# Kernel optimization log

Measured on AMD Instinct MI355X. Metric: run time of the kernel, lower is better.

The kernel has to match this reference:

```python
import jax, jax.numpy as jnp
import numpy as np

B_COEF = 0.1          # position-offset scale 'b'
STRIDE = (1, 1)
PADDING = (1, 1)


def setup_inputs() -> dict:
    key = jax.random.key(0)
    k1, k2, k3 = jax.random.split(key, 3)
    x = jax.random.normal(k1, (16, 64, 128, 128), dtype=jnp.float32)
    kernel = jax.random.normal(k2, (128, 64, 3, 3), dtype=jnp.float32)
    bias = jax.random.normal(k3, (128,), dtype=jnp.float32)
    return {"x": x, "kernel": kernel, "bias": bias}


def _conv(inp, w):
    pads = [(PADDING[0], PADDING[0]), (PADDING[1], PADDING[1])]
    return jax.lax.conv_general_dilated(
        inp, w, window_strides=STRIDE, padding=pads,
        dimension_numbers=("NCHW", "OIHW", "NCHW"))


def reference(x, kernel, bias):
    # out[b,o,p] = sum_i x_unf[b,i,p] * (kernel_flat[o,i] + b*grid[p]) + bias[o]
    # = conv(x, kernel) + b*grid[p] * sum_i x_unf[b,i,p] + bias  (rank-1 separable)
    kh, kw = kernel.shape[2], kernel.shape[3]
    main = _conv(x, kernel)                                  # (B, O, Ho, Wo)
    H_out, W_out = main.shape[2], main.shape[3]

    # sum over in_channels and kernel window = ones-conv of channel-summed input
    ones_k = jnp.ones((1, 1, kh, kw), dtype=x.dtype)
    patch_sum = _conv(x.sum(axis=1, keepdims=True), ones_k)  # (B, 1, Ho, Wo)

    # Replicate torch meshgrid(arange(W_out), arange(H_out), indexing='ij')
    # -> flatten (W,H) row-major -> consumed as (H,W) row-major by the view.
    gx = jnp.arange(W_out)[:, None] + jnp.arange(H_out)[None, :]  # (Wo, Ho)
    grid2d = gx.reshape(-1).reshape(H_out, W_out).astype(x.dtype)  # (Ho, Wo)

    return main + B_COEF * grid2d * patch_sum + bias[None, :, None, None]
```

## Files before the change

### kernel.cpp

```cpp
#include <hip/hip_runtime.h>
#include <hip/hip_bf16.h>


typedef __attribute__((ext_vector_type(8))) short short8;
typedef __attribute__((ext_vector_type(4))) float f32x4;

#define B_COEF 0.1f
constexpr int CI = 64, CO = 128, H = 128, W = 128;
constexpr int SH = 4;
constexpr int XPAD = 72;

static __device__ inline short bf16s(float v) {
    __hip_bfloat16 b = __float2bfloat16(v);
    return *reinterpret_cast<short*>(&b);
}

static __device__ inline void bar_lgkm() {
    asm volatile("s_waitcnt lgkmcnt(0)" ::: "memory");
    __builtin_amdgcn_s_barrier();
    asm volatile("" ::: "memory");
}
static __device__ inline void bar_plain() {
    asm volatile("" ::: "memory");
    __builtin_amdgcn_s_barrier();
    asm volatile("" ::: "memory");
}


__global__ void prep_wq(const float* __restrict__ wgt, __hip_bfloat16* __restrict__ wq) {
    int idx = blockIdx.x * 256 + threadIdx.x;
    if (idx < 9 * CO * CI) {
        int tap = idx >> 13;
        int rem = idx & 8191;
        int oc = rem >> 6, ci = rem & 63;
        int kc = ci >> 5, j = ci & 31;
        wq[(((tap * 2 + kc) * CO + oc) << 5) + j] =
            __float2bfloat16(wgt[(oc * CI + ci) * 9 + tap]);
    }
}

static __device__ __forceinline__ void loadrow(const float* __restrict__ xb, int r,
                                               int wl, int cg0, float* pf) {
    if ((unsigned)r < (unsigned)H) {
        const float* px = xb + (size_t)r * W + wl;
#pragma unroll
        for (int p = 0; p < 4; ++p) {
            const int cg = cg0 + 2 * p;
#pragma unroll
            for (int j = 0; j < 8; ++j)
                pf[p * 8 + j] = px[(size_t)(cg * 8 + j) * (H * W)];
        }
    } else {
#pragma unroll
        for (int i = 0; i < 32; ++i) pf[i] = 0.0f;
    }
}

static __device__ __forceinline__ void writerow(__hip_bfloat16* __restrict__ xs,
                                                float* __restrict__ psb, int tid,
                                                int wslot, int cg0, const float* pf) {
    const int wsw = wslot & 7;
    float part = 0.0f;
#pragma unroll
    for (int p = 0; p < 4; ++p) {
        const int cg = cg0 + 2 * p;
        short8 pk;
#pragma unroll
        for (int j = 0; j < 8; ++j) {
            pk[j] = bf16s(pf[p * 8 + j]);
            part += pf[p * 8 + j];
        }
        *(short8*)&xs[wslot * 64 + ((cg ^ wsw) * 8)] = pk;
    }
    psb[tid] = part;
}

__global__ __launch_bounds__(256, 2)
void conv_fused(const float* __restrict__ x,
                const __hip_bfloat16* __restrict__ wq,
                const float* __restrict__ bias,
                float* __restrict__ out) {
    __shared__ __hip_bfloat16 xrow[3][130 * 64];
    __shared__ float Srow[3][132];
    __shared__ float ps3[132];
    __shared__ float psb[256];

    const int tid = threadIdx.x, bx = blockIdx.x, b = blockIdx.y;
    const int u = ((bx & 7) << 2) | (bx >> 3);
    const int h0 = u * SH;
    const int lane = tid & 63, waveid = tid >> 6;
    const int lo16 = lane & 15, quad = lane >> 4;
    const int m0 = (waveid & 1) * 64, n0 = (waveid >> 1) * 64;
    const int wl = tid & 127, cg0 = tid >> 7, wslot = wl + 1;

    const float* xb = x + (size_t)b * CI * H * W;

    if (tid < 48) {
        const int sl = tid >> 4, col = (tid & 8) ? 129 : 0, uu = tid & 7;
        short8 z = {0, 0, 0, 0, 0, 0, 0, 0};
        *(short8*)&xrow[sl][col * 64 + ((uu ^ (col & 7)) * 8)] = z;
    }
    if (tid == 48) ps3[0] = 0.0f;
    if (tid == 49) ps3[129] = 0.0f;

#pragma unroll
    for (int k = 0; k < 2; ++k) {
        const int r = h0 - 1 + k;
        float pf[32];
        loadrow(xb, r, wl, cg0, pf);
        writerow(&xrow[(r + 1) % 3][0], psb, tid, wslot, cg0, pf);
        bar_lgkm();
        if (tid < 128) Srow[(r + 1) % 3][tid + 1] = psb[tid] + psb[tid + 128];
        bar_lgkm();
    }
    {
        float pf[32];
        loadrow(xb, h0 + 1, wl, cg0, pf);
        writerow(&xrow[(h0 + 2) % 3][0], psb, tid, wslot, cg0, pf);
        bar_lgkm();
    }

    for (int t = 0; t < SH; ++t) {
        const int h = h0 + t;

        float pf[32];
        if (t < SH - 1) loadrow(xb, h + 2, wl, cg0, pf);

        if (tid < 128) {
            const float v = psb[tid] + psb[tid + 128];
            Srow[(h + 2) % 3][tid + 1] = v;
            ps3[tid + 1] = Srow[h % 3][tid + 1] + Srow[(h + 1) % 3][tid + 1] + v;
        }
        bar_lgkm();

        f32x4 acc[4][4] = {};
        __builtin_amdgcn_s_setprio(1);
#pragma unroll
        for (int kh = 0; kh < 3; ++kh) {
            const __hip_bfloat16* xs = &xrow[(h + kh) % 3][0];
#pragma unroll
            for (int kw = 0; kw < 3; ++kw) {
                const int tap = kh * 3 + kw;
                short8 bq[2][4];
#pragma unroll
                for (int kc = 0; kc < 2; ++kc)
#pragma unroll
                    for (int ni = 0; ni < 4; ++ni)
                        bq[kc][ni] = *(const short8*)(
                            wq + (((tap * 2 + kc) * CO + n0 + ni * 16 + lo16) << 5) + quad * 8);
#pragma unroll
                for (int kc = 0; kc < 2; ++kc) {
                    short8 af[4];
#pragma unroll
                    for (int mi = 0; mi < 4; ++mi) {
                        const int row = m0 + mi * 16 + lo16 + kw;
                        af[mi] = *(const short8*)
                            &xs[row * 64 + (((kc * 4 + quad) ^ (row & 7)) * 8)];
                    }
#pragma unroll
                    for (int mi = 0; mi < 4; ++mi)
#pragma unroll
                        for (int ni = 0; ni < 4; ++ni)
                            acc[mi][ni] = __builtin_amdgcn_mfma_f32_16x16x32_bf16(
                                af[mi], bq[kc][ni], acc[mi][ni], 0, 0, 0);
                }
            }
        }
        __builtin_amdgcn_s_setprio(0);

#pragma unroll
        for (int mi = 0; mi < 4; ++mi) {
            const int wbase = m0 + mi * 16 + quad * 4;
            float cs[6];
#pragma unroll
            for (int q2 = 0; q2 < 6; ++q2) cs[q2] = ps3[wbase + q2];
            float ps[4], cf[4];
#pragma unroll
            for (int q2 = 0; q2 < 4; ++q2) {
                ps[q2] = cs[q2] + cs[q2 + 1] + cs[q2 + 2];
                cf[q2] = B_COEF * (float)(h + wbase + q2);
            }
#pragma unroll
            for (int ni = 0; ni < 4; ++ni) {
                const int oc = n0 + ni * 16 + lo16;
                const float bv = bias[oc];
                f32x4 v = acc[mi][ni];
#pragma unroll
                for (int q2 = 0; q2 < 4; ++q2) v[q2] = v[q2] + cf[q2] * ps[q2] + bv;
                *(f32x4*)(out + (((size_t)b * CO + oc) * H + h) * W + wbase) = v;
            }
        }
        bar_plain();

        if (t < SH - 1) {
            writerow(&xrow[h % 3][0], psb, tid, wslot, cg0, pf);
            bar_lgkm();
        }
    }
}


constexpr int WPAD = 72;

__global__ void prep_w_fb(const float* __restrict__ wgt, __hip_bfloat16* __restrict__ wt) {
    int idx = blockIdx.x * 256 + threadIdx.x;
    if (idx < 9 * CO * CI) {
        int tap = idx / (CO * CI);
        int rem = idx - tap * (CO * CI);
        int oc = rem >> 6, ci = rem & 63;
        wt[idx] = __float2bfloat16(wgt[(oc * CI + ci) * 9 + tap]);
    }
}

__global__ __launch_bounds__(256, 2)
void conv_fb(const float* __restrict__ x, const __hip_bfloat16* __restrict__ wt,
             const float* __restrict__ bias, float* __restrict__ out) {
    __shared__ __hip_bfloat16 xrow[130 * XPAD];
    __shared__ __hip_bfloat16 wlds[CO * WPAD];
    __shared__ float colsum[132];

    const int tid = threadIdx.x;
    const int h = blockIdx.x, b = blockIdx.y;
    const int lane = tid & 63, waveid = tid >> 6;
    const int lo16 = lane & 15, quad = lane >> 4;
    const int m0 = (waveid & 1) * 64, n0 = (waveid >> 1) * 64;

    f32x4 acc[4][4] = {};
    if (tid < 132) colsum[tid] = 0.0f;
    const float* xb = x + (size_t)b * CI * H * W;

    const int w16 = tid & 15, cipl = (tid >> 4) & 3, rest0 = tid >> 6;

    for (int kh = 0; kh < 3; ++kh) {
        const int gh = h - 1 + kh;
        __syncthreads();
        for (int it = 0; it < 18; ++it) {
            int rest = rest0 + it * 4;
            int whi = rest % 9, ciph = rest / 9;
            int w = whi * 16 + w16;
            int ci0 = (ciph * 4 + cipl) * 2;
            int gw = w - 1;
            float x0 = 0.0f, x1 = 0.0f;
            if (w < 130 && gw >= 0 && gw < W && gh >= 0 && gh < H) {
                const float* p = xb + (size_t)ci0 * (H * W) + gh * W + gw;
                x0 = p[0];
                x1 = p[H * W];
            }
            if (w < 130) {
                __hip_bfloat162 pk;
                pk.x = __float2bfloat16(x0);
                pk.y = __float2bfloat16(x1);
                *(__hip_bfloat162*)&xrow[w * XPAD + ci0] = pk;
            }
            float cs = x0 + x1;
            cs += __shfl_xor(cs, 16);
            cs += __shfl_xor(cs, 32);
            if (quad == 0 && w < 130) atomicAdd(&colsum[w], cs);
        }
        for (int kw = 0; kw < 3; ++kw) {
            __syncthreads();
            {
                const __hip_bfloat16* wtap = wt + (kh * 3 + kw) * (CO * CI);
#pragma unroll
                for (int it = 0; it < 4; ++it) {
                    int j = tid + it * 256;
                    int oc = j >> 3, ch = (j & 7) * 8;
                    short8 v = *(const short8*)(wtap + oc * CI + ch);
                    *(short8*)&wlds[oc * WPAD + ch] = v;
                }
            }
            __syncthreads();
#pragma unroll
            for (int kc = 0; kc < 2; ++kc) {
                const int krow = kc * 32 + quad * 8;
                short8 af[4], bf[4];
#pragma unroll
                for (int mi = 0; mi < 4; ++mi)
                    af[mi] = *(const short8*)&xrow[(m0 + mi * 16 + lo16 + kw) * XPAD + krow];
#pragma unroll
                for (int ni = 0; ni < 4; ++ni)
                    bf[ni] = *(const short8*)&wlds[(n0 + ni * 16 + lo16) * WPAD + krow];
#pragma unroll
                for (int mi = 0; mi < 4; ++mi)
#pragma unroll
                    for (int ni = 0; ni < 4; ++ni)
                        acc[mi][ni] = __builtin_amdgcn_mfma_f32_16x16x32_bf16(
                            af[mi], bf[ni], acc[mi][ni], 0, 0, 0);
            }
        }
    }
    __syncthreads();
#pragma unroll
    for (int mi = 0; mi < 4; ++mi) {
        const int wbase = m0 + mi * 16 + quad * 4;
        float cs[6];
#pragma unroll
        for (int r = 0; r < 6; ++r) cs[r] = colsum[wbase + r];
        float ps[4], cf[4];
#pragma unroll
        for (int r = 0; r < 4; ++r) {
            ps[r] = cs[r] + cs[r + 1] + cs[r + 2];
            cf[r] = B_COEF * (float)(h + wbase + r);
        }
#pragma unroll
        for (int ni = 0; ni < 4; ++ni) {
            const int oc = n0 + ni * 16 + lo16;
            const float bv = bias[oc];
            f32x4 v = acc[mi][ni];
#pragma unroll
            for (int r = 0; r < 4; ++r) v[r] = v[r] + cf[r] * ps[r] + bv;
            *(f32x4*)(out + (((size_t)b * CO + oc) * H + h) * W + wbase) = v;
        }
    }
}


extern "C" void kernel_launch(void* const* d_in, const int* in_sizes, int n_in,
                              void* d_out, int out_size, void* d_ws, size_t ws_size,
                              hipStream_t stream) {
    const float* x    = (const float*)d_in[0];
    const float* wgt  = (const float*)d_in[1];
    const float* bias = (const float*)d_in[2];
    float* out = (float*)d_out;

    const size_t WQ_BYTES = (size_t)9 * 2 * CO * 32 * 2;

    if (ws_size >= WQ_BYTES) {
        __hip_bfloat16* wq = (__hip_bfloat16*)d_ws;
        prep_wq<<<dim3(288), dim3(256), 0, stream>>>(wgt, wq);
        conv_fused<<<dim3(H / SH, 16), dim3(256), 0, stream>>>(x, wq, bias, out);
    } else {
        __hip_bfloat16* wt = (__hip_bfloat16*)d_ws;
        prep_w_fb<<<dim3(288), dim3(256), 0, stream>>>(wgt, wt);
        conv_fb<<<dim3(H, 16), dim3(256), 0, stream>>>(x, wt, bias, out);
    }
}
```

Baseline: 258.2 us.

## Double workgroup width, split output channels per wave, and deepen row-buffer pipeline

```diff
diff --git a/kernel.cpp b/kernel.cpp
--- a/kernel.cpp
+++ b/kernel.cpp
@@ -17,11 +17,6 @@
 
 static __device__ inline void bar_lgkm() {
     asm volatile("s_waitcnt lgkmcnt(0)" ::: "memory");
-    __builtin_amdgcn_s_barrier();
-    asm volatile("" ::: "memory");
-}
-static __device__ inline void bar_plain() {
-    asm volatile("" ::: "memory");
     __builtin_amdgcn_s_barrier();
     asm volatile("" ::: "memory");
 }
@@ -40,112 +35,115 @@
 }
 
 static __device__ __forceinline__ void loadrow(const float* __restrict__ xb, int r,
-                                               int wl, int cg0, float* pf) {
+                                               int wl, int u0, float* pf) {
     if ((unsigned)r < (unsigned)H) {
         const float* px = xb + (size_t)r * W + wl;
 #pragma unroll
-        for (int p = 0; p < 4; ++p) {
-            const int cg = cg0 + 2 * p;
+        for (int uu = 0; uu < 2; ++uu)
 #pragma unroll
             for (int j = 0; j < 8; ++j)
-                pf[p * 8 + j] = px[(size_t)(cg * 8 + j) * (H * W)];
-        }
+                pf[uu * 8 + j] = px[(size_t)((u0 + uu) * 8 + j) * (H * W)];
     } else {
 #pragma unroll
-        for (int i = 0; i < 32; ++i) pf[i] = 0.0f;
+        for (int i = 0; i < 16; ++i) pf[i] = 0.0f;
     }
 }
 
 static __device__ __forceinline__ void writerow(__hip_bfloat16* __restrict__ xs,
                                                 float* __restrict__ psb, int tid,
-                                                int wslot, int cg0, const float* pf) {
+                                                int wslot, int u0, const float* pf) {
     const int wsw = wslot & 7;
     float part = 0.0f;
 #pragma unroll
-    for (int p = 0; p < 4; ++p) {
-        const int cg = cg0 + 2 * p;
+    for (int uu = 0; uu < 2; ++uu) {
         short8 pk;
 #pragma unroll
         for (int j = 0; j < 8; ++j) {
-            pk[j] = bf16s(pf[p * 8 + j]);
-            part += pf[p * 8 + j];
-        }
-        *(short8*)&xs[wslot * 64 + ((cg ^ wsw) * 8)] = pk;
+            pk[j] = bf16s(pf[uu * 8 + j]);
+            part += pf[uu * 8 + j];
+        }
+        *(short8*)&xs[wslot * 64 + (((u0 + uu) ^ wsw) * 8)] = pk;
     }
     psb[tid] = part;
 }
 
-__global__ __launch_bounds__(256, 2)
+__global__ __launch_bounds__(512, 2)
 void conv_fused(const float* __restrict__ x,
                 const __hip_bfloat16* __restrict__ wq,
                 const float* __restrict__ bias,
                 float* __restrict__ out) {
-    __shared__ __hip_bfloat16 xrow[3][130 * 64];
-    __shared__ float Srow[3][132];
+    __shared__ __hip_bfloat16 xrow[4][130 * 64];
+    __shared__ float Srow[4][132];
     __shared__ float ps3[132];
-    __shared__ float psb[256];
+    __shared__ float psb[512];
 
     const int tid = threadIdx.x, bx = blockIdx.x, b = blockIdx.y;
     const int u = ((bx & 7) << 2) | (bx >> 3);
     const int h0 = u * SH;
     const int lane = tid & 63, waveid = tid >> 6;
     const int lo16 = lane & 15, quad = lane >> 4;
-    const int m0 = (waveid & 1) * 64, n0 = (waveid >> 1) * 64;
-    const int wl = tid & 127, cg0 = tid >> 7, wslot = wl + 1;
+    const int m0 = (waveid & 1) * 64, n0 = (waveid >> 1) * 32;
+    const int wl = tid & 127, u0 = (tid >> 7) * 2, wslot = wl + 1;
 
     const float* xb = x + (size_t)b * CI * H * W;
 
-    if (tid < 48) {
+    if (tid < 64) {
         const int sl = tid >> 4, col = (tid & 8) ? 129 : 0, uu = tid & 7;
         short8 z = {0, 0, 0, 0, 0, 0, 0, 0};
         *(short8*)&xrow[sl][col * 64 + ((uu ^ (col & 7)) * 8)] = z;
     }
-    if (tid == 48) ps3[0] = 0.0f;
-    if (tid == 49) ps3[129] = 0.0f;
-
-#pragma unroll
-    for (int k = 0; k < 2; ++k) {
+    if (tid == 64) ps3[0] = 0.0f;
+    if (tid == 65) ps3[129] = 0.0f;
+
+    float pr0[16], pr1[16], pr2[16], pfA[16], pfB[16];
+    loadrow(xb, h0 - 1, wl, u0, pr0);
+    loadrow(xb, h0,     wl, u0, pr1);
+    loadrow(xb, h0 + 1, wl, u0, pr2);
+    loadrow(xb, h0 + 2, wl, u0, pfA);
+#pragma unroll
+    for (int k = 0; k < 3; ++k) {
         const int r = h0 - 1 + k;
-        float pf[32];
-        loadrow(xb, r, wl, cg0, pf);
-        writerow(&xrow[(r + 1) % 3][0], psb, tid, wslot, cg0, pf);
+        const float* pk = (k == 0) ? pr0 : (k == 1) ? pr1 : pr2;
+        writerow(&xrow[(r + 1) & 3][0], psb, tid, wslot, u0, pk);
         bar_lgkm();
-        if (tid < 128) Srow[(r + 1) % 3][tid + 1] = psb[tid] + psb[tid + 128];
+        if (tid < 128)
+            Srow[(r + 1) & 3][tid + 1] =
+                psb[tid] + psb[tid + 128] + psb[tid + 256] + psb[tid + 384];
         bar_lgkm();
     }
-    {
-        float pf[32];
-        loadrow(xb, h0 + 1, wl, cg0, pf);
-        writerow(&xrow[(h0 + 2) % 3][0], psb, tid, wslot, cg0, pf);
-        bar_lgkm();
-    }
-
+
+#pragma unroll
     for (int t = 0; t < SH; ++t) {
         const int h = h0 + t;
 
-        float pf[32];
-        if (t < SH - 1) loadrow(xb, h + 2, wl, cg0, pf);
-
-        if (tid < 128) {
-            const float v = psb[tid] + psb[tid + 128];
-            Srow[(h + 2) % 3][tid + 1] = v;
-            ps3[tid + 1] = Srow[h % 3][tid + 1] + Srow[(h + 1) % 3][tid + 1] + v;
-        }
+        if (t == 0) loadrow(xb, h0 + 3, wl, u0, pfB);
+        if (t == 1) loadrow(xb, h0 + 4, wl, u0, pfA);
+
+        if (tid < 128)
+            ps3[tid + 1] = Srow[h & 3][tid + 1] + Srow[(h + 1) & 3][tid + 1] +
+                           Srow[(h + 2) & 3][tid + 1];
+
+        if (t < 3)
+            writerow(&xrow[(h + 3) & 3][0], psb, tid, wslot, u0,
+                     (t & 1) ? pfB : pfA);
         bar_lgkm();
-
-        f32x4 acc[4][4] = {};
+        if (t < 3 && tid < 128)
+            Srow[(h + 3) & 3][tid + 1] =
+                psb[tid] + psb[tid + 128] + psb[tid + 256] + psb[tid + 384];
+
+        f32x4 acc[4][2] = {};
         __builtin_amdgcn_s_setprio(1);
 #pragma unroll
         for (int kh = 0; kh < 3; ++kh) {
-            const __hip_bfloat16* xs = &xrow[(h + kh) % 3][0];
+            const __hip_bfloat16* xs = &xrow[(h + kh) & 3][0];
 #pragma unroll
             for (int kw = 0; kw < 3; ++kw) {
                 const int tap = kh * 3 + kw;
-                short8 bq[2][4];
+                short8 bq[2][2];
 #pragma unroll
                 for (int kc = 0; kc < 2; ++kc)
 #pragma unroll
-                    for (int ni = 0; ni < 4; ++ni)
+                    for (int ni = 0; ni < 2; ++ni)
                         bq[kc][ni] = *(const short8*)(
                             wq + (((tap * 2 + kc) * CO + n0 + ni * 16 + lo16) << 5) + quad * 8);
 #pragma unroll
@@ -160,7 +158,7 @@
 #pragma unroll
                     for (int mi = 0; mi < 4; ++mi)
 #pragma unroll
-                        for (int ni = 0; ni < 4; ++ni)
+                        for (int ni = 0; ni < 2; ++ni)
                             acc[mi][ni] = __builtin_amdgcn_mfma_f32_16x16x32_bf16(
                                 af[mi], bq[kc][ni], acc[mi][ni], 0, 0, 0);
                 }
@@ -181,7 +179,7 @@
                 cf[q2] = B_COEF * (float)(h + wbase + q2);
             }
 #pragma unroll
-            for (int ni = 0; ni < 4; ++ni) {
+            for (int ni = 0; ni < 2; ++ni) {
                 const int oc = n0 + ni * 16 + lo16;
                 const float bv = bias[oc];
                 f32x4 v = acc[mi][ni];
@@ -190,12 +188,7 @@
                 *(f32x4*)(out + (((size_t)b * CO + oc) * H + h) * W + wbase) = v;
             }
         }
-        bar_plain();
-
-        if (t < SH - 1) {
-            writerow(&xrow[h % 3][0], psb, tid, wslot, cg0, pf);
-            bar_lgkm();
-        }
+        if (t < SH - 1) bar_lgkm();
     }
 }
 
@@ -328,7 +321,7 @@
     if (ws_size >= WQ_BYTES) {
         __hip_bfloat16* wq = (__hip_bfloat16*)d_ws;
         prep_wq<<<dim3(288), dim3(256), 0, stream>>>(wgt, wq);
-        conv_fused<<<dim3(H / SH, 16), dim3(256), 0, stream>>>(x, wq, bias, out);
+        conv_fused<<<dim3(H / SH, 16), dim3(512), 0, stream>>>(x, wq, bias, out);
     } else {
         __hip_bfloat16* wt = (__hip_bfloat16*)d_ws;
         prep_w_fb<<<dim3(288), dim3(256), 0, stream>>>(wgt, wt);
```

Result: faster. 234.4 us (-9.2%).
